# Performance work log

Measured on AMD Instinct MI355X. Metric: run time of the kernel, lower is better.

Reference implementation:

```python
import jax, jax.numpy as jnp
import numpy as np

B, S, H, NH, K = 8, 1024, 1024, 16, 512
HD = H // NH  # head dim = 64


def setup_inputs() -> dict:
    key = jax.random.key(0)
    ks = jax.random.split(key, 9)
    hidden_states = jax.random.normal(ks[0], (B, S, H), jnp.float32)
    # remain_layers: exactly K nonzero entries per row (static max_tokens = K)
    scores = jax.random.uniform(ks[1], (B, S))
    thresh = jnp.sort(scores, axis=1)[:, S - K][:, None]
    remain_layers = (scores >= thresh).astype(jnp.int32)
    attention_mask = jnp.zeros((B, 1, 1, S), jnp.float32)  # additive mask
    init = 0.02
    Wq = jax.random.normal(ks[2], (H, H), jnp.float32) * init
    bq = jnp.zeros((H,), jnp.float32)
    Wk = jax.random.normal(ks[3], (H, H), jnp.float32) * init
    bk = jnp.zeros((H,), jnp.float32)
    Wv = jax.random.normal(ks[4], (H, H), jnp.float32) * init
    bv = jnp.zeros((H,), jnp.float32)
    return {"hidden_states": hidden_states, "attention_mask": attention_mask,
            "remain_layers": remain_layers, "Wq": Wq, "bq": bq,
            "Wk": Wk, "bk": bk, "Wv": Wv, "bv": bv}


def _heads(x):  # [B, L, H] -> [B, NH, L, HD]
    b, l, _ = x.shape
    return x.reshape(b, l, NH, HD).transpose(0, 2, 1, 3)


def reference(hidden_states, attention_mask, remain_layers, Wq, bq, Wk, bk, Wv, bv):
    # get_reduced_hidden: per-row gather of tokens with remain_layers > 0,
    # in original position order, zero-padded to max_tokens (= K here).
    order = jnp.argsort(1 - remain_layers, axis=1, stable=True)  # nonzeros first, order kept
    idx = order[:, :K]                                           # [B, K]
    reduced = jnp.take_along_axis(hidden_states, idx[:, :, None], axis=1)  # [B, K, H]
    valid = (jnp.take_along_axis(remain_layers, idx, axis=1) > 0)
    reduced = reduced * valid[:, :, None].astype(reduced.dtype)  # zero-pad slots

    q = _heads(reduced @ Wq.T + bq)          # [B, NH, K, HD]
    k = _heads(hidden_states @ Wk.T + bk)    # [B, NH, S, HD]
    v = _heads(hidden_states @ Wv.T + bv)    # [B, NH, S, HD]

    scores = jnp.einsum('bhqd,bhkd->bhqk', q, k) / np.sqrt(HD).astype(np.float32)
    scores = scores + attention_mask         # additive mask broadcast
    probs = jax.nn.softmax(scores, axis=-1)  # dropout is identity at eval
    ctx = jnp.einsum('bhqk,bhkd->bhqd', probs, v)  # [B, NH, K, HD]
    ctx = ctx.transpose(0, 2, 1, 3).reshape(B, K, H)
    return ctx
```

## Files before the change

kernel.cpp:

```cpp
#include <hip/hip_runtime.h>
#include <hip/hip_bf16.h>
#include <stdint.h>

#define S_LEN 1024
#define HDIM  1024
#define NHEADS 16
#define HEAD_D 64
#define KSEL  512
#define BATCH 8

typedef unsigned short ushort_t;
typedef __attribute__((ext_vector_type(8))) __bf16 bf16x8;
typedef __attribute__((ext_vector_type(4))) float  f32x4;

typedef const __attribute__((address_space(1))) void cg_void;
typedef __attribute__((address_space(3))) void lds_void;

__device__ __forceinline__ void gl_lds16(const void* g, void* l) {
    __builtin_amdgcn_global_load_lds((cg_void*)g, (lds_void*)l, 16, 0, 0);
}

__device__ __forceinline__ ushort_t f2bf(float f) {
    union { float f; unsigned int i; } x; x.f = f;
    unsigned int r = (x.i + 0x7fffu + ((x.i >> 16) & 1u)) >> 16;
    return (ushort_t)r;
}

__global__ void cvt_all(const float* __restrict__ hidden, const float* __restrict__ wq,
                        const float* __restrict__ wk, const float* __restrict__ wv,
                        ushort_t* __restrict__ hbf, ushort_t* __restrict__ wqb,
                        ushort_t* __restrict__ wkb, ushort_t* __restrict__ wvb) {
    int blk = blockIdx.x;
    const float* s; ushort_t* d; int base;
    if (blk < 8192)       { s = hidden; d = hbf; base = blk; }
    else if (blk < 9216)  { s = wq; d = wqb; base = blk - 8192; }
    else if (blk < 10240) { s = wk; d = wkb; base = blk - 9216; }
    else                  { s = wv; d = wvb; base = blk - 10240; }
    int i = base * 256 + threadIdx.x;
    float4 v = ((const float4*)s)[i];
    ushort4 o;
    o.x = f2bf(v.x); o.y = f2bf(v.y); o.z = f2bf(v.z); o.w = f2bf(v.w);
    ((ushort4*)d)[i] = o;
}

__global__ void compact_kernel(const int* __restrict__ remain,
                               int* __restrict__ idx, int* __restrict__ valid) {
    int b = blockIdx.x, t = threadIdx.x;
    int r = remain[b * S_LEN + t];
    unsigned long long m = __ballot(r != 0);
    int lane = t & 63, w = t >> 6;
    __shared__ int wsum[16];
    __shared__ int woff[17];
    int pre = __popcll(m & ((1ull << lane) - 1ull));
    if (lane == 0) wsum[w] = __popcll(m);
    __syncthreads();
    if (t == 0) { int a = 0; for (int i = 0; i < 16; i++) { woff[i] = a; a += wsum[i]; } woff[16] = a; }
    __syncthreads();
    int tot = woff[16];
    int onesBefore = woff[w] + pre;
    int slot = r ? onesBefore : (tot + (t - onesBefore));
    if (slot < KSEL) { idx[b * KSEL + slot] = t; valid[b * KSEL + slot] = r; }
}

#define QSCALE 0.1803368801111244f
#define LT_PITCH 136
__global__ __launch_bounds__(256, 2) void gemm_fused(
    const ushort_t* __restrict__ hbf, const ushort_t* __restrict__ wkv,
    const ushort_t* __restrict__ wq,
    const float* __restrict__ bk, const float* __restrict__ bv,
    const float* __restrict__ bq,
    const int* __restrict__ idx, const int* __restrict__ valid,
    ushort_t* __restrict__ kp, ushort_t* __restrict__ vt, ushort_t* __restrict__ qp) {
    const int z = blockIdx.z;
    if (z == 1 && (blockIdx.x >= 8 || blockIdx.y >= 32)) return;
    __shared__ __align__(16) ushort_t pool[128 * LT_PITCH];
    ushort_t* As = pool;
    ushort_t* Bs = pool + 4096;
    const int tid = threadIdx.x;
    const int lane = tid & 63;
    const int w = tid >> 6;
    const int quad = lane >> 4;
    const int cl = lane & 15;
    const long bm = (long)blockIdx.y * 128;
    const int bn = blockIdx.x * 128;
    const int srow = w * 16 + (lane >> 2);
    const int scol = (lane & 3) * 8;
    const int lds_off = w * 512 + lane * 8;
    const int wr = (w >> 1) * 64, wc = (w & 1) * 64;

    const ushort_t* W = z ? wq : wkv;

    long ab[2];
#pragma unroll
    for (int p = 0; p < 2; p++) {
        long gr = bm + p * 64 + srow;
        if (z == 0) ab[p] = gr * HDIM;
        else {
            int b_ = (int)(gr >> 9);
            int src = idx[(b_ << 9) + ((int)gr & 511)];
            ab[p] = ((long)(b_ << 10) + src) * HDIM;
        }
    }

    f32x4 acc[4][4] = {};

    for (int k0 = 0; k0 < HDIM; k0 += 32) {
#pragma unroll
        for (int p = 0; p < 2; p++) {
            gl_lds16(hbf + ab[p] + k0 + scol, &As[p * 2048 + lds_off]);
            gl_lds16(W + ((long)(bn + p * 64 + srow)) * HDIM + k0 + scol, &Bs[p * 2048 + lds_off]);
        }
        __syncthreads();
        bf16x8 af[4], bfr[4];
#pragma unroll
        for (int mt = 0; mt < 4; mt++)
            af[mt] = *(const bf16x8*)&As[(wr + mt * 16 + cl) * 32 + quad * 8];
#pragma unroll
        for (int nt = 0; nt < 4; nt++)
            bfr[nt] = *(const bf16x8*)&Bs[(wc + nt * 16 + cl) * 32 + quad * 8];
#pragma unroll
        for (int mt = 0; mt < 4; mt++)
#pragma unroll
            for (int nt = 0; nt < 4; nt++)
                acc[mt][nt] = __builtin_amdgcn_mfma_f32_16x16x32_bf16(af[mt], bfr[nt], acc[mt][nt], 0, 0, 0);
        __syncthreads();
    }

    if (z == 1) {
#pragma unroll
        for (int nt = 0; nt < 4; nt++) {
            int col = bn + wc + nt * 16 + cl;
            float bvq = bq[col];
#pragma unroll
            for (int mt = 0; mt < 4; mt++) {
                long row = bm + wr + mt * 16 + quad * 4;
#pragma unroll
                for (int r = 0; r < 4; r++) {
                    float vm = (float)valid[row + r];
                    qp[(row + r) * HDIM + col] = f2bf((acc[mt][nt][r] * vm + bvq) * QSCALE);
                }
            }
        }
    } else if (bn < 1024) {
#pragma unroll
        for (int nt = 0; nt < 4; nt++) {
            int col = bn + wc + nt * 16 + cl;
            float bvk = bk[col];
#pragma unroll
            for (int mt = 0; mt < 4; mt++) {
                long row = bm + wr + mt * 16 + quad * 4;
#pragma unroll
                for (int r = 0; r < 4; r++)
                    kp[(row + r) * HDIM + col] = f2bf(acc[mt][nt][r] + bvk);
            }
        }
    } else {
        ushort_t* Lt = pool;
#pragma unroll
        for (int nt = 0; nt < 4; nt++) {
            int col = wc + nt * 16 + cl;
            float bvv = bv[bn - 1024 + col];
#pragma unroll
            for (int mt = 0; mt < 4; mt++) {
                int row0 = wr + mt * 16 + quad * 4;
#pragma unroll
                for (int r = 0; r < 4; r++)
                    Lt[col * LT_PITCH + row0 + r] = f2bf(acc[mt][nt][r] + bvv);
            }
        }
        __syncthreads();
        int vtRow = tid >> 1, half = tid & 1;
        long b_ = bm >> 10, s0 = bm & 1023;
        long gbase = ((b_ << 10) + (bn - 1024) + vtRow) * 1024 + s0 + half * 64;
        const ushort_t* src = Lt + vtRow * LT_PITCH + half * 64;
#pragma unroll
        for (int i = 0; i < 8; i++)
            *(bf16x8*)(vt + gbase + i * 8) = *(const bf16x8*)(src + i * 8);
    }
}

#define P_PITCH 72
__global__ __launch_bounds__(512, 4) void attn_kernel(
    const ushort_t* __restrict__ qp, const ushort_t* __restrict__ kp,
    const ushort_t* __restrict__ vt, const float* __restrict__ mask,
    float* __restrict__ out) {
    __shared__ __align__(16) ushort_t ks[2][2 * 64 * 32];
    __shared__ __align__(16) ushort_t vs[2][2 * 64 * 32];
    __shared__ __align__(16) ushort_t ps[8][16 * P_PITCH];
    const int tid = threadIdx.x;
    const int lane = tid & 63;
    const int w = tid >> 6;
    const int quad = lane >> 4;
    const int cl = lane & 15;
    const int qt = blockIdx.x, h = blockIdx.y, b = blockIdx.z;

    const int skk = tid >> 8;
    const int ss  = (tid & 255) >> 2;
    const int sc8 = (tid & 3) * 8;
    const int lds_off = tid * 8;

    const long kbase = (long)b * S_LEN;
    const long vbase = (long)b * 1024 + h * HEAD_D;

    const long qrow = (long)b * KSEL + qt * 128 + w * 16 + cl;
    bf16x8 aq[2];
#pragma unroll
    for (int kk = 0; kk < 2; kk++)
        aq[kk] = *(const bf16x8*)(qp + qrow * HDIM + h * HEAD_D + kk * 32 + quad * 8);

    f32x4 O[4] = {};
    float l_r[4] = {0.f, 0.f, 0.f, 0.f};

    gl_lds16(kp + (kbase + ss) * (long)HDIM + h * HEAD_D + skk * 32 + sc8, &ks[0][lds_off]);
    gl_lds16(vt + (vbase + ss) * (long)S_LEN + skk * 32 + sc8, &vs[0][lds_off]);

    for (int c = 0; c < S_LEN / 64; c++) {
        __asm__ volatile("s_waitcnt vmcnt(0)" ::: "memory");
        __syncthreads();
        if (c + 1 < S_LEN / 64) {
            int nb = (c + 1) & 1;
            gl_lds16(kp + (kbase + (c + 1) * 64 + ss) * (long)HDIM + h * HEAD_D + skk * 32 + sc8,
                     &ks[nb][lds_off]);
            gl_lds16(vt + (vbase + ss) * (long)S_LEN + (c + 1) * 64 + skk * 32 + sc8,
                     &vs[nb][lds_off]);
        }
        const ushort_t* kbuf = ks[c & 1];
        const ushort_t* vbuf = vs[c & 1];

        f32x4 sc[4] = {};
#pragma unroll
        for (int kk = 0; kk < 2; kk++) {
#pragma unroll
            for (int nt = 0; nt < 4; nt++) {
                bf16x8 bk8 = *(const bf16x8*)&kbuf[kk * 2048 + (nt * 16 + cl) * 32 + quad * 8];
                sc[nt] = __builtin_amdgcn_mfma_f32_16x16x32_bf16(aq[kk], bk8, sc[nt], 0, 0, 0);
            }
        }
#pragma unroll
        for (int nt = 0; nt < 4; nt++) {
            float mv = mask[b * S_LEN + c * 64 + nt * 16 + cl] * 1.44269504f;
#pragma unroll
            for (int r = 0; r < 4; r++) {
                float p_ = __builtin_amdgcn_exp2f(sc[nt][r] + mv);
                sc[nt][r] = p_;
                l_r[r] += p_;
            }
        }

#pragma unroll
        for (int nt = 0; nt < 4; nt++)
#pragma unroll
            for (int r = 0; r < 4; r++)
                ps[w][(quad * 4 + r) * P_PITCH + nt * 16 + cl] = f2bf(sc[nt][r]);

        __asm__ volatile("s_waitcnt lgkmcnt(0)" ::: "memory");

#pragma unroll
        for (int kk = 0; kk < 2; kk++) {
            bf16x8 ap = *(const bf16x8*)&ps[w][cl * P_PITCH + kk * 32 + quad * 8];
#pragma unroll
            for (int dt = 0; dt < 4; dt++) {
                bf16x8 bv8 = *(const bf16x8*)&vbuf[kk * 2048 + (dt * 16 + cl) * 32 + quad * 8];
                O[dt] = __builtin_amdgcn_mfma_f32_16x16x32_bf16(ap, bv8, O[dt], 0, 0, 0);
            }
        }
    }

#pragma unroll
    for (int r = 0; r < 4; r++) {
        float s0 = l_r[r];
#pragma unroll
        for (int d = 1; d < 16; d <<= 1) s0 += __shfl_xor(s0, d, 64);
        l_r[r] = s0;
    }

    const long orow0 = (long)b * KSEL + qt * 128 + w * 16 + quad * 4;
#pragma unroll
    for (int dt = 0; dt < 4; dt++) {
        int col = h * HEAD_D + dt * 16 + cl;
#pragma unroll
        for (int r = 0; r < 4; r++)
            out[(orow0 + r) * HDIM + col] = O[dt][r] / l_r[r];
    }
}

extern "C" void kernel_launch(void* const* d_in, const int* in_sizes, int n_in,
                              void* d_out, int out_size, void* d_ws, size_t ws_size,
                              hipStream_t stream) {
    const float* hidden = (const float*)d_in[0];
    const float* mask   = (const float*)d_in[1];
    const int*   remain = (const int*)d_in[2];
    const float* Wq = (const float*)d_in[3];
    const float* bq = (const float*)d_in[4];
    const float* Wk = (const float*)d_in[5];
    const float* bk = (const float*)d_in[6];
    const float* Wv = (const float*)d_in[7];
    const float* bv = (const float*)d_in[8];
    float* out = (float*)d_out;

    char* ws = (char*)d_ws;
    size_t off = 0;
    int* idx   = (int*)(ws + off); off += 16384;
    int* valid = (int*)(ws + off); off += 16384;
    ushort_t* hbf = (ushort_t*)(ws + off); off += (size_t)BATCH * S_LEN * HDIM * 2;
    ushort_t* wqb = (ushort_t*)(ws + off); off += (size_t)HDIM * HDIM * 2;
    ushort_t* wkb = (ushort_t*)(ws + off); off += (size_t)HDIM * HDIM * 2;
    ushort_t* wvb = (ushort_t*)(ws + off); off += (size_t)HDIM * HDIM * 2;
    ushort_t* qp  = (ushort_t*)(ws + off); off += (size_t)BATCH * KSEL * HDIM * 2;
    ushort_t* kp  = (ushort_t*)(ws + off); off += (size_t)BATCH * S_LEN * HDIM * 2;
    ushort_t* vt  = (ushort_t*)(ws + off); off += (size_t)BATCH * S_LEN * HDIM * 2;

    cvt_all<<<11264, 256, 0, stream>>>(hidden, Wq, Wk, Wv, hbf, wqb, wkb, wvb);
    compact_kernel<<<BATCH, 1024, 0, stream>>>(remain, idx, valid);
    gemm_fused<<<dim3(16, 64, 2), 256, 0, stream>>>(hbf, wkb, wqb, bk, bv, bq,
                                                    idx, valid, kp, vt, qp);
    attn_kernel<<<dim3(4, NHEADS, BATCH), 512, 0, stream>>>(qp, kp, vt, mask, out);
}
```

Before: 205.6 us.

## Merge prep kernels, compact GEMM grid with swizzle, shrink LDS for higher occupancy

Fuses the bf16 conversion and token compaction into a single 1024-thread launch, removing one kernel launch. The GEMM grid becomes a flat 1D grid with no early-exit blocks for the Q projection, and its block-to-tile mapping is reordered so consecutive blocks reuse the same weight tiles. The shared-memory pool is halved by writing the V transpose in two 64-column passes, and launch bounds are raised to 5 blocks per CU. The trade-off is extra barriers in the V epilogue and tighter register limits that could cause spills.

Result: slower. 221.6 us (+7.8%).

```diff
diff --git a/kernel.cpp b/kernel.cpp
--- a/kernel.cpp
+++ b/kernel.cpp
@@ -26,63 +26,68 @@
     return (ushort_t)r;
 }
 
-__global__ void cvt_all(const float* __restrict__ hidden, const float* __restrict__ wq,
-                        const float* __restrict__ wk, const float* __restrict__ wv,
-                        ushort_t* __restrict__ hbf, ushort_t* __restrict__ wqb,
-                        ushort_t* __restrict__ wkb, ushort_t* __restrict__ wvb) {
-    int blk = blockIdx.x;
-    const float* s; ushort_t* d; int base;
-    if (blk < 8192)       { s = hidden; d = hbf; base = blk; }
-    else if (blk < 9216)  { s = wq; d = wqb; base = blk - 8192; }
-    else if (blk < 10240) { s = wk; d = wkb; base = blk - 9216; }
-    else                  { s = wv; d = wvb; base = blk - 10240; }
-    int i = base * 256 + threadIdx.x;
-    float4 v = ((const float4*)s)[i];
-    ushort4 o;
-    o.x = f2bf(v.x); o.y = f2bf(v.y); o.z = f2bf(v.z); o.w = f2bf(v.w);
-    ((ushort4*)d)[i] = o;
-}
-
-__global__ void compact_kernel(const int* __restrict__ remain,
-                               int* __restrict__ idx, int* __restrict__ valid) {
-    int b = blockIdx.x, t = threadIdx.x;
-    int r = remain[b * S_LEN + t];
-    unsigned long long m = __ballot(r != 0);
-    int lane = t & 63, w = t >> 6;
+__global__ __launch_bounds__(1024) void prep_kernel(
+    const float* __restrict__ hidden, const float* __restrict__ wq,
+    const float* __restrict__ wk, const float* __restrict__ wv,
+    const int* __restrict__ remain,
+    ushort_t* __restrict__ hbf, ushort_t* __restrict__ wqb,
+    ushort_t* __restrict__ wkb, ushort_t* __restrict__ wvb,
+    int* __restrict__ idx, int* __restrict__ valid) {
     __shared__ int wsum[16];
     __shared__ int woff[17];
-    int pre = __popcll(m & ((1ull << lane) - 1ull));
-    if (lane == 0) wsum[w] = __popcll(m);
-    __syncthreads();
-    if (t == 0) { int a = 0; for (int i = 0; i < 16; i++) { woff[i] = a; a += wsum[i]; } woff[16] = a; }
-    __syncthreads();
-    int tot = woff[16];
-    int onesBefore = woff[w] + pre;
-    int slot = r ? onesBefore : (tot + (t - onesBefore));
-    if (slot < KSEL) { idx[b * KSEL + slot] = t; valid[b * KSEL + slot] = r; }
+    int blk = blockIdx.x;
+    if (blk < 2816) {
+        const float* s; ushort_t* d; int base;
+        if (blk < 2048)      { s = hidden; d = hbf; base = blk; }
+        else if (blk < 2304) { s = wq; d = wqb; base = blk - 2048; }
+        else if (blk < 2560) { s = wk; d = wkb; base = blk - 2304; }
+        else                 { s = wv; d = wvb; base = blk - 2560; }
+        int i = base * 1024 + threadIdx.x;
+        float4 v = ((const float4*)s)[i];
+        ushort4 o;
+        o.x = f2bf(v.x); o.y = f2bf(v.y); o.z = f2bf(v.z); o.w = f2bf(v.w);
+        ((ushort4*)d)[i] = o;
+    } else {
+        int b = blk - 2816, t = threadIdx.x;
+        int r = remain[b * S_LEN + t];
+        unsigned long long m = __ballot(r != 0);
+        int lane = t & 63, w = t >> 6;
+        int pre = __popcll(m & ((1ull << lane) - 1ull));
+        if (lane == 0) wsum[w] = __popcll(m);
+        __syncthreads();
+        if (t == 0) { int a = 0; for (int i = 0; i < 16; i++) { woff[i] = a; a += wsum[i]; } woff[16] = a; }
+        __syncthreads();
+        int tot = woff[16];
+        int onesBefore = woff[w] + pre;
+        int slot = r ? onesBefore : (tot + (t - onesBefore));
+        if (slot < KSEL) { idx[b * KSEL + slot] = t; valid[b * KSEL + slot] = r; }
+    }
 }
 
 #define QSCALE 0.1803368801111244f
 #define LT_PITCH 136
-__global__ __launch_bounds__(256, 2) void gemm_fused(
+__global__ __launch_bounds__(256, 5) void gemm_fused(
     const ushort_t* __restrict__ hbf, const ushort_t* __restrict__ wkv,
     const ushort_t* __restrict__ wq,
     const float* __restrict__ bk, const float* __restrict__ bv,
     const float* __restrict__ bq,
     const int* __restrict__ idx, const int* __restrict__ valid,
     ushort_t* __restrict__ kp, ushort_t* __restrict__ vt, ushort_t* __restrict__ qp) {
-    const int z = blockIdx.z;
-    if (z == 1 && (blockIdx.x >= 8 || blockIdx.y >= 32)) return;
-    __shared__ __align__(16) ushort_t pool[128 * LT_PITCH];
+    __shared__ __align__(16) ushort_t pool[64 * LT_PITCH];
     ushort_t* As = pool;
     ushort_t* Bs = pool + 4096;
+    const int i = blockIdx.x;
+    int z, bmI, bnI;
+    if (i < 1024) { z = 0; int x = i & 7, j = i >> 3; bmI = x * 8 + (j >> 4); bnI = j & 15; }
+    else          { z = 1; int q = i - 1024;          bmI = q >> 3;           bnI = q & 7;  }
+    const long bm = (long)bmI * 128;
+    const int bn = bnI * 128;
+
     const int tid = threadIdx.x;
     const int lane = tid & 63;
     const int w = tid >> 6;
     const int quad = lane >> 4;
     const int cl = lane & 15;
-    const long bm = (long)blockIdx.y * 128;
-    const int bn = blockIdx.x * 128;
     const int srow = w * 16 + (lane >> 2);
     const int scol = (lane & 3) * 8;
     const int lds_off = w * 512 + lane * 8;
@@ -156,26 +161,32 @@
         }
     } else {
         ushort_t* Lt = pool;
-#pragma unroll
-        for (int nt = 0; nt < 4; nt++) {
-            int col = wc + nt * 16 + cl;
-            float bvv = bv[bn - 1024 + col];
-#pragma unroll
-            for (int mt = 0; mt < 4; mt++) {
-                int row0 = wr + mt * 16 + quad * 4;
-#pragma unroll
-                for (int r = 0; r < 4; r++)
-                    Lt[col * LT_PITCH + row0 + r] = f2bf(acc[mt][nt][r] + bvv);
-            }
-        }
-        __syncthreads();
-        int vtRow = tid >> 1, half = tid & 1;
         long b_ = bm >> 10, s0 = bm & 1023;
-        long gbase = ((b_ << 10) + (bn - 1024) + vtRow) * 1024 + s0 + half * 64;
-        const ushort_t* src = Lt + vtRow * LT_PITCH + half * 64;
-#pragma unroll
-        for (int i = 0; i < 8; i++)
-            *(bf16x8*)(vt + gbase + i * 8) = *(const bf16x8*)(src + i * 8);
+#pragma unroll
+        for (int p2 = 0; p2 < 2; p2++) {
+            if ((w & 1) == p2) {
+#pragma unroll
+                for (int nt = 0; nt < 4; nt++) {
+                    int cloc = nt * 16 + cl;
+                    float bvv = bv[bn - 1024 + p2 * 64 + cloc];
+#pragma unroll
+                    for (int mt = 0; mt < 4; mt++) {
+                        int row0 = wr + mt * 16 + quad * 4;
+#pragma unroll
+                        for (int r = 0; r < 4; r++)
+                            Lt[cloc * LT_PITCH + row0 + r] = f2bf(acc[mt][nt][r] + bvv);
+                    }
+                }
+            }
+            __syncthreads();
+            int c2 = tid >> 2, quarter = tid & 3;
+            long gbase = ((b_ << 10) + (bn - 1024) + p2 * 64 + c2) * 1024 + s0 + quarter * 32;
+            const ushort_t* src = Lt + c2 * LT_PITCH + quarter * 32;
+#pragma unroll
+            for (int q8 = 0; q8 < 4; q8++)
+                *(bf16x8*)(vt + gbase + q8 * 8) = *(const bf16x8*)(src + q8 * 8);
+            __syncthreads();
+        }
     }
 }
 
@@ -310,9 +321,9 @@
     ushort_t* kp  = (ushort_t*)(ws + off); off += (size_t)BATCH * S_LEN * HDIM * 2;
     ushort_t* vt  = (ushort_t*)(ws + off); off += (size_t)BATCH * S_LEN * HDIM * 2;
 
-    cvt_all<<<11264, 256, 0, stream>>>(hidden, Wq, Wk, Wv, hbf, wqb, wkb, wvb);
-    compact_kernel<<<BATCH, 1024, 0, stream>>>(remain, idx, valid);
-    gemm_fused<<<dim3(16, 64, 2), 256, 0, stream>>>(hbf, wkb, wqb, bk, bv, bq,
-                                                    idx, valid, kp, vt, qp);
+    prep_kernel<<<2824, 1024, 0, stream>>>(hidden, Wq, Wk, Wv, remain,
+                                           hbf, wqb, wkb, wvb, idx, valid);
+    gemm_fused<<<1280, 256, 0, stream>>>(hbf, wkb, wqb, bk, bv, bq,
+                                         idx, valid, kp, vt, qp);
     attn_kernel<<<dim3(4, NHEADS, BATCH), 512, 0, stream>>>(qp, kp, vt, mask, out);
 }
```
